# Optimization experiments

Measured on AMD Instinct MI355X. Metric: run time of the kernel, lower is better.

The kernel has to match this reference:

```python
import jax, jax.numpy as jnp
import numpy as np

L = 3          # num encoder layers
H = 128        # hidden_dim
NH = 8         # num_heads
HD = H // NH   # head_dim
FF = H * 4     # ff inner dim (after GLU)
B, N = 32, 512
NUM_BINS = 50


def _linear_params(key, fan_in, fan_out):
    kw, kb = jax.random.split(key)
    lim = 1.0 / np.sqrt(fan_in)
    W = jax.random.uniform(kw, (fan_in, fan_out), jnp.float32, -lim, lim)
    b = jax.random.uniform(kb, (fan_out,), jnp.float32, -lim, lim)
    return W, b


def setup_inputs() -> dict:
    key = jax.random.key(0)
    ks = jax.random.split(key, 16)
    x = jax.random.normal(ks[0], (B, N, H), jnp.float32)
    distance_matrix = jax.random.uniform(ks[1], (B, N, N), jnp.float32)
    mask = jax.random.randint(ks[2], (B, N), 0, 2).astype(bool)

    def stack_linear(k, fan_in, fan_out):
        Ws, bs = [], []
        for l in range(L):
            W, b = _linear_params(jax.random.fold_in(k, l), fan_in, fan_out)
            Ws.append(W); bs.append(b)
        return jnp.stack(Ws), jnp.stack(bs)

    Wq, bq = stack_linear(ks[3], H, H)
    Wk, bk = stack_linear(ks[4], H, H)
    Wv, bv = stack_linear(ks[5], H, H)
    Wo, bo = stack_linear(ks[6], H, H)
    dist_emb = jax.random.normal(ks[7], (L, NUM_BINS, NH), jnp.float32)
    attn_bias = jnp.zeros((L, NH, 1, 1), jnp.float32)
    g1 = jnp.ones((L, H), jnp.float32); b1 = jnp.zeros((L, H), jnp.float32)
    g2 = jnp.ones((L, H), jnp.float32); b2 = jnp.zeros((L, H), jnp.float32)
    Wf1, bf1 = stack_linear(ks[8], H, 2 * FF)
    Wf2, bf2 = stack_linear(ks[9], FF, H)
    return dict(x=x, distance_matrix=distance_matrix, mask=mask,
                Wq=Wq, bq=bq, Wk=Wk, bk=bk, Wv=Wv, bv=bv, Wo=Wo, bo=bo,
                dist_emb=dist_emb, attn_bias=attn_bias,
                g1=g1, b1=b1, g2=g2, b2=b2,
                Wf1=Wf1, bf1=bf1, Wf2=Wf2, bf2=bf2)


def _layernorm(x, g, b, eps=1e-5):
    mu = jnp.mean(x, axis=-1, keepdims=True)
    var = jnp.var(x, axis=-1, keepdims=True)
    return (x - mu) * jax.lax.rsqrt(var + eps) * g + b


def _attention(h, bins, key_mask, Wq, bq, Wk, bk, Wv, bv, Wo, bo, dist_emb, attn_bias):
    # h: [B,N,H]; bins: [B,N,N] int; key_mask: [B,N] bool (True = masked)
    Bsz, Nn, _ = h.shape
    Q = (h @ Wq + bq).reshape(Bsz, Nn, NH, HD)
    K = (h @ Wk + bk).reshape(Bsz, Nn, NH, HD)
    V = (h @ Wv + bv).reshape(Bsz, Nn, NH, HD)
    scores = jnp.einsum('bqhd,bkhd->bhqk', Q, K) / np.sqrt(HD)
    bias = jnp.transpose(dist_emb[bins], (0, 3, 1, 2))  # [B,NH,N,N]
    scores = scores + bias + attn_bias[None]
    scores = jnp.where(key_mask[:, None, None, :], -1e9, scores)
    attn = jax.nn.softmax(scores, axis=-1)
    out = jnp.einsum('bhqk,bkhd->bqhd', attn, V).reshape(Bsz, Nn, H)
    return out @ Wo + bo


def reference(x, distance_matrix, mask, Wq, bq, Wk, bk, Wv, bv, Wo, bo,
              dist_emb, attn_bias, g1, b1, g2, b2, Wf1, bf1, Wf2, bf2):
    bins = jnp.clip((distance_matrix * 10.0).astype(jnp.int32), 0, NUM_BINS - 1)
    h = x
    for l in range(L):
        # pre-LN attention block
        a = _attention(_layernorm(h, g1[l], b1[l]), bins, mask,
                       Wq[l], bq[l], Wk[l], bk[l], Wv[l], bv[l], Wo[l], bo[l],
                       dist_emb[l], attn_bias[l])
        h = h + a
        # pre-LN GLU feed-forward
        u = _layernorm(h, g2[l], b2[l]) @ Wf1[l] + bf1[l]  # [B,N,2*FF]
        ua, ub = jnp.split(u, 2, axis=-1)
        h = h + (ua * jax.nn.sigmoid(ub)) @ Wf2[l] + bf2[l]
    return h
```

## Files before the change

kernel.cpp:

```cpp
#include <hip/hip_runtime.h>
#include <stdint.h>

#define Bq 32
#define Nq 512
#define Hq 128
#define NHq 8
#define HDq 16
#define Mq (Bq * Nq)

typedef unsigned short u16;
typedef __attribute__((ext_vector_type(8))) short short8;
typedef __attribute__((ext_vector_type(8))) _Float16 half8;
typedef __attribute__((ext_vector_type(2))) __fp16 fp16x2;
typedef __attribute__((ext_vector_type(4))) float f32x4;

__device__ __forceinline__ float bf2f(u16 v) {
    return __uint_as_float(((unsigned int)v) << 16);
}
__device__ __forceinline__ float ldin(const void* p, long idx, int bf) {
    if (bf) return bf2f(((const u16*)p)[idx]);
    return ((const float*)p)[idx];
}
__device__ __forceinline__ u16 f2bf(float v) {
    unsigned int u = __float_as_uint(v);
    return (u16)((u + 0x7FFFu + ((u >> 16) & 1u)) >> 16);
}
__device__ __forceinline__ u16 f2h(float v) {
    _Float16 h = (_Float16)v;
    return *(u16*)&h;
}
__device__ __forceinline__ unsigned pk2h(float a, float b) {
    fp16x2 c = __builtin_amdgcn_cvt_pkrtz(a, b);
    return *(unsigned*)&c;
}

__global__ void prep_kernel(const void* xraw, const void* de, const void* ab,
                            const void* mraw, int* flag, float* deo, float* abo,
                            unsigned* mbits, int n) {
    __shared__ int cnt, orA, orB, orC, orD;
    int tid = threadIdx.x;
    if (tid == 0) { cnt = 0; orA = 0; orB = 0; orC = 0; orD = 0; }
    __syncthreads();
    const u16* u = (const u16*)xraw;
    int good = 0;
    for (int i = tid; i < 1024; i += 256) {
        u16 v = u[i];
        int e = (v >> 7) & 0xFF;
        if (v == 0 || (e >= 90 && e <= 141)) good++;
    }
    atomicAdd(&cnt, good);
    const uint4* p4 = (const uint4*)mraw;
    unsigned a = 0, b = 0, c = 0, d = 0;
    for (int i = tid; i < n / 16; i += 256) {
        uint4 w = p4[i];
        unsigned all = w.x | w.y | w.z | w.w;
        a |= all & 0xFEFEFEFEu;
        b |= all & 0x0000FF00u;
        c |= all & 0xFFFFFF00u;
        d |= w.y | w.w;
    }
    if (a) atomicOr(&orA, 1);
    if (b) atomicOr(&orB, 1);
    if (c) atomicOr(&orC, 1);
    if (d) atomicOr(&orD, 1);
    __syncthreads();
    int bf = (cnt >= 900);
    if (tid == 0) *flag = bf;
    int mode;
    if (orA) mode = orB ? 3 : 4;
    else if (orC) mode = 0;
    else mode = orD ? 1 : 2;
    for (int i = tid; i < 1200; i += 256) deo[i] = ldin(de, i, bf);
    if (tid < 24) abo[tid] = ldin(ab, tid, bf);
    const unsigned char* p = (const unsigned char*)mraw;
    for (int wI = tid; wI < n / 32; wI += 256) {
        unsigned word = 0;
        for (int j = 0; j < 32; ++j) {
            int i = wI * 32 + j;
            int v;
            switch (mode) {
                case 0: v = p[i]; break;
                case 1: v = ((const int*)p)[i]; break;
                case 2: v = (int)((const long long*)p)[i]; break;
                case 3: v = ((const u16*)p)[i] != 0; break;
                default: v = (((const float*)p)[i] != 0.0f); break;
            }
            if (v) word |= 1u << j;
        }
        mbits[wI] = word;
    }
}

__global__ void kprep_kernel(const unsigned* __restrict__ mbits,
                             u16* __restrict__ kidxg, int* __restrict__ nkt,
                             unsigned* __restrict__ tmask) {
    int b = blockIdx.x;
    int lane = threadIdx.x & 63;
    int pos_base = 0;
    for (int w = 0; w < 8; ++w) {
        unsigned lo = mbits[b * 16 + 2 * w], hi = mbits[b * 16 + 2 * w + 1];
        unsigned long long word = ((unsigned long long)hi << 32) | lo;
        unsigned long long un = ~word;
        int bit = (int)((un >> lane) & 1ull);
        unsigned long long before = un & ((1ull << lane) - 1ull);
        int pos = pos_base + __popcll(before);
        if (bit) kidxg[b * 512 + pos] = (u16)(w * 64 + lane);
        pos_base += __popcll(un);
    }
    int nk = pos_base;
    int nkp = (nk + 31) & ~31;
    if (nkp == 0) nkp = 32;
    int nt = nkp >> 5;
    for (int j = nk + lane; j < nkp; j += 64) kidxg[b * 512 + j] = 0;
    if (lane == 0) {
        nkt[b] = nt;
        for (int t = 0; t < 16; ++t) tmask[b * 16 + t] = 0;
        int rem = nk & 31;
        if (rem) tmask[b * 16 + nt - 1] = 0xFFFFFFFFu << rem;
        if (nk == 0) tmask[b * 16] = 0xFFFFFFFFu;
    }
}

__global__ __launch_bounds__(256) void binsc_kernel(
    const void* __restrict__ dist, const u16* __restrict__ kidxg,
    const int* __restrict__ nkt, unsigned char* __restrict__ binsc,
    const int* flagp) {
    int bf = *flagp;
    int b = blockIdx.y;
    int q0 = blockIdx.x * 8;
    __shared__ u16 kl[512];
    __shared__ int ntS;
    int tid = threadIdx.x;
    if (tid == 0) ntS = nkt[b];
    kl[tid] = kidxg[b * 512 + tid];
    kl[tid + 256] = kidxg[b * 512 + tid + 256];
    __syncthreads();
    int nkp = ntS * 32;
    for (int rq = 0; rq < 8; ++rq) {
        int q = q0 + rq;
        long rowoff = ((long)b * 512 + q) * 512;
        for (int j = tid; j < nkp; j += 256) {
            float d = ldin(dist, rowoff + kl[j], bf);
            int v = (int)(d * 10.0f);
            v = v < 0 ? 0 : (v > 49 ? 49 : v);
            binsc[((size_t)b * 512 + q) * 512 + j] = (unsigned char)(v << 2);
        }
    }
}

__global__ __launch_bounds__(256) void init_ln_kernel(
    const void* x, float* __restrict__ h, u16* __restrict__ hn,
    const void* graw, const void* braw, const int* flagp) {
    int bf = *flagp;
    int row = blockIdx.x * 4 + (threadIdx.x >> 6);
    int lane = threadIdx.x & 63;
    float x0 = ldin(x, (long)row * Hq + lane, bf);
    float x1 = ldin(x, (long)row * Hq + lane + 64, bf);
    h[(size_t)row * Hq + lane] = x0;
    h[(size_t)row * Hq + lane + 64] = x1;
    float s = x0 + x1, s2 = x0 * x0 + x1 * x1;
#pragma unroll
    for (int o = 32; o; o >>= 1) {
        s += __shfl_xor(s, o);
        s2 += __shfl_xor(s2, o);
    }
    float mu = s * (1.0f / 128.0f);
    float var = fmaxf(s2 * (1.0f / 128.0f) - mu * mu, 0.0f);
    float rr = rsqrtf(var + 1e-5f);
    float g0 = ldin(graw, lane, bf), g1v = ldin(graw, lane + 64, bf);
    float b0 = ldin(braw, lane, bf), b1v = ldin(braw, lane + 64, bf);
    hn[(size_t)row * Hq + lane]      = f2bf((x0 - mu) * rr * g0 + b0);
    hn[(size_t)row * Hq + lane + 64] = f2bf((x1 - mu) * rr * g1v + b1v);
}

__global__ __launch_bounds__(256) void wtrans_kernel(
    const void* Wqr, const void* Wkr, const void* Wvr, const void* Wor,
    const void* Wf1r, const void* Wf2r,
    u16* qkvT, u16* oT, u16* f1T, u16* f2T, const int* flagp) {
    int bf = *flagp;
    int bid = blockIdx.x;
    int l = bid >> 8, r = bid & 255;
    const void* src; u16* dst; long soff, doff; int Kd, Nd, t;
    if (r < 64) {
        int mat = r >> 4; t = r & 15; Kd = 128; Nd = 128;
        soff = (long)l * 16384;
        if (mat == 0)      { src = Wqr; dst = qkvT; doff = (long)l * 49152; }
        else if (mat == 1) { src = Wkr; dst = qkvT; doff = (long)l * 49152 + 16384; }
        else if (mat == 2) { src = Wvr; dst = qkvT; doff = (long)l * 49152 + 32768; }
        else               { src = Wor; dst = oT;   doff = (long)l * 16384; }
    } else if (r < 192) {
        t = r - 64; Kd = 128; Nd = 1024;
        src = Wf1r; soff = (long)l * 131072; dst = f1T; doff = (long)l * 131072;
    } else {
        t = r - 192; Kd = 512; Nd = 128;
        src = Wf2r; soff = (long)l * 65536; dst = f2T; doff = (long)l * 65536;
    }
    int ntile = Nd >> 5;
    int tk = t / ntile, tn = t % ntile;
    __shared__ u16 Ts[32][33];
    int rr = threadIdx.x >> 3, cc0 = (threadIdx.x & 7) * 4;
#pragma unroll
    for (int i = 0; i < 4; ++i) {
        long idx = soff + (long)(tk * 32 + rr) * Nd + tn * 32 + cc0 + i;
        Ts[rr][cc0 + i] = f2bf(ldin(src, idx, bf));
    }
    __syncthreads();
#pragma unroll
    for (int i = 0; i < 4; ++i) {
        long idx = doff + (long)(tn * 32 + rr) * Kd + tk * 32 + cc0 + i;
        dst[idx] = Ts[cc0 + i][rr];
    }
}

__global__ __launch_bounds__(256, 2) void mfma_gemm64_kernel(
    const u16* __restrict__ A, const u16* __restrict__ WT,
    const void* __restrict__ braw, long bOff, float* __restrict__ C,
    int K, int resid, const int* flagp,
    const void* lnG, const void* lnB, long lnOff, u16* hnout, void* outp) {
    __shared__ __align__(16) u16 As[64][40];
    __shared__ __align__(16) u16 Bs[128][40];
    __shared__ float Ct[64][128];
    int tid = threadIdx.x;
    int m0 = blockIdx.x * 64;
    int wave = tid >> 6, lane = tid & 63;
    int wm = (wave >> 1) * 32, wn = (wave & 1) * 64;
    int q = lane >> 4, ln = lane & 15;
    f32x4 zero = {0.f, 0.f, 0.f, 0.f};
    f32x4 acc[2][4];
#pragma unroll
    for (int i = 0; i < 2; ++i)
#pragma unroll
        for (int j = 0; j < 4; ++j) acc[i][j] = zero;
    int sar = tid >> 2, sac = (tid & 3) * 8;
    int sbr = tid >> 1, sbc = (tid & 1) * 16;
    const u16* Ap = A + (size_t)(m0 + sar) * K + sac;
    const u16* Bp = WT + (size_t)sbr * K + sbc;
    for (int k0 = 0; k0 < K; k0 += 32) {
        uint4 av = *(const uint4*)(Ap + k0);
        uint4 b0 = *(const uint4*)(Bp + k0);
        uint4 b1 = *(const uint4*)(Bp + k0 + 8);
        *(uint4*)&As[sar][sac] = av;
        *(uint4*)&Bs[sbr][sbc] = b0; *(uint4*)&Bs[sbr][sbc + 8] = b1;
        __syncthreads();
        short8 af[2], bfv[4];
#pragma unroll
        for (int t = 0; t < 2; ++t) af[t] = *(const short8*)&As[wm + t * 16 + ln][q * 8];
#pragma unroll
        for (int t = 0; t < 4; ++t) bfv[t] = *(const short8*)&Bs[wn + t * 16 + ln][q * 8];
#pragma unroll
        for (int ti = 0; ti < 2; ++ti)
#pragma unroll
            for (int tj = 0; tj < 4; ++tj)
                acc[ti][tj] = __builtin_amdgcn_mfma_f32_16x16x32_bf16(
                    af[ti], bfv[tj], acc[ti][tj], 0, 0, 0);
        __syncthreads();
    }
    int bf = *flagp;
#pragma unroll
    for (int tj = 0; tj < 4; ++tj) {
        int n = wn + tj * 16 + ln;
        float bias = ldin(braw, bOff + n, bf);
#pragma unroll
        for (int ti = 0; ti < 2; ++ti)
#pragma unroll
            for (int r = 0; r < 4; ++r) {
                int m = m0 + wm + ti * 16 + q * 4 + r;
                float v = acc[ti][tj][r] + bias;
                float* dst = C + (size_t)m * 128 + n;
                if (resid) v += *dst;
                *dst = v;
                Ct[m - m0][n] = v;
                if (outp) {
                    if (bf) ((u16*)outp)[(size_t)m * 128 + n] = f2bf(v);
                    else ((float*)outp)[(size_t)m * 128 + n] = v;
                }
            }
    }
    if (hnout) {
        __syncthreads();
        float gg0 = ldin(lnG, lnOff + lane, bf);
        float gg1 = ldin(lnG, lnOff + lane + 64, bf);
        float bb0 = ldin(lnB, lnOff + lane, bf);
        float bb1 = ldin(lnB, lnOff + lane + 64, bf);
        for (int rr = 0; rr < 16; ++rr) {
            int row = wave * 16 + rr;
            float x0 = Ct[row][lane], x1 = Ct[row][lane + 64];
            float s = x0 + x1, s2v = x0 * x0 + x1 * x1;
#pragma unroll
            for (int o = 32; o; o >>= 1) {
                s += __shfl_xor(s, o);
                s2v += __shfl_xor(s2v, o);
            }
            float mu = s * (1.0f / 128.0f);
            float var = fmaxf(s2v * (1.0f / 128.0f) - mu * mu, 0.0f);
            float rstd = rsqrtf(var + 1e-5f);
            int m = m0 + row;
            hnout[(size_t)m * 128 + lane]      = f2bf((x0 - mu) * rstd * gg0 + bb0);
            hnout[(size_t)m * 128 + lane + 64] = f2bf((x1 - mu) * rstd * gg1 + bb1);
        }
    }
}

__global__ __launch_bounds__(256, 2) void qkv_mfma_kernel(
    const u16* __restrict__ A, const u16* __restrict__ qkvT_l,
    const void* bqr, const void* bkr, const void* bvr, long bOff,
    u16* __restrict__ Qo, u16* __restrict__ Ko, u16* __restrict__ Vo,
    const int* flagp) {
    int sel = blockIdx.y;
    const u16* WT = qkvT_l + (size_t)sel * 16384;
    const void* braw = sel == 0 ? bqr : (sel == 1 ? bkr : bvr);
    u16* C = sel == 0 ? Qo : (sel == 1 ? Ko : Vo);
    float scale = sel == 0 ? 0.25f : 1.0f;
    __shared__ __align__(16) u16 As[64][40];
    __shared__ __align__(16) u16 Bs[128][40];
    int tid = threadIdx.x;
    int m0 = blockIdx.x * 64;
    int wave = tid >> 6, lane = tid & 63;
    int wm = (wave >> 1) * 32, wn = (wave & 1) * 64;
    int q = lane >> 4, ln = lane & 15;
    f32x4 zero = {0.f, 0.f, 0.f, 0.f};
    f32x4 acc[2][4];
#pragma unroll
    for (int i = 0; i < 2; ++i)
#pragma unroll
        for (int j = 0; j < 4; ++j) acc[i][j] = zero;
    int sar = tid >> 2, sac = (tid & 3) * 8;
    int sbr = tid >> 1, sbc = (tid & 1) * 16;
    const u16* Ap = A + (size_t)(m0 + sar) * 128 + sac;
    const u16* Bp = WT + (size_t)sbr * 128 + sbc;
#pragma unroll
    for (int k0 = 0; k0 < 128; k0 += 32) {
        uint4 av = *(const uint4*)(Ap + k0);
        uint4 b0 = *(const uint4*)(Bp + k0);
        uint4 b1 = *(const uint4*)(Bp + k0 + 8);
        *(uint4*)&As[sar][sac] = av;
        *(uint4*)&Bs[sbr][sbc] = b0; *(uint4*)&Bs[sbr][sbc + 8] = b1;
        __syncthreads();
        short8 af[2], bfv[4];
#pragma unroll
        for (int t = 0; t < 2; ++t) af[t] = *(const short8*)&As[wm + t * 16 + ln][q * 8];
#pragma unroll
        for (int t = 0; t < 4; ++t) bfv[t] = *(const short8*)&Bs[wn + t * 16 + ln][q * 8];
#pragma unroll
        for (int ti = 0; ti < 2; ++ti)
#pragma unroll
            for (int tj = 0; tj < 4; ++tj)
                acc[ti][tj] = __builtin_amdgcn_mfma_f32_16x16x32_bf16(
                    af[ti], bfv[tj], acc[ti][tj], 0, 0, 0);
        __syncthreads();
    }
    int bf = *flagp;
#pragma unroll
    for (int tj = 0; tj < 4; ++tj) {
        int n = wn + tj * 16 + ln;
        float bias = ldin(braw, bOff + n, bf);
#pragma unroll
        for (int ti = 0; ti < 2; ++ti)
#pragma unroll
            for (int r = 0; r < 4; ++r) {
                int m = m0 + wm + ti * 16 + q * 4 + r;
                C[(size_t)m * 128 + n] = f2h((acc[ti][tj][r] + bias) * scale);
            }
    }
}

__global__ __launch_bounds__(256, 2) void glu_mfma_kernel(
    const u16* __restrict__ A, const u16* __restrict__ f1T_l,
    const void* __restrict__ braw, long bOff, u16* __restrict__ Vout,
    const int* flagp) {
    __shared__ __align__(16) u16 As[128][40];
    __shared__ __align__(16) u16 Ba[64][40];
    __shared__ __align__(16) u16 Bb[64][40];
    int tid = threadIdx.x;
    int m0 = blockIdx.x * 128, n0 = blockIdx.y * 64;
    int wave = tid >> 6, lane = tid & 63;
    int wm = (wave >> 1) * 64, wn = (wave & 1) * 32;
    int q = lane >> 4, ln = lane & 15;
    f32x4 zero = {0.f, 0.f, 0.f, 0.f};
    f32x4 accA[4][2], accB[4][2];
#pragma unroll
    for (int i = 0; i < 4; ++i)
#pragma unroll
        for (int j = 0; j < 2; ++j) { accA[i][j] = zero; accB[i][j] = zero; }
    int sr = tid >> 1, sc = (tid & 1) * 16;
    const u16* Ap = A + (size_t)(m0 + sr) * 128 + sc;
    const u16* BpA = f1T_l + (size_t)(n0 + sr) * 128 + sc;
    const u16* BpB = f1T_l + (size_t)(512 + n0 + (sr - 64)) * 128 + sc;
#pragma unroll
    for (int k0 = 0; k0 < 128; k0 += 32) {
        uint4 a0 = *(const uint4*)(Ap + k0);
        uint4 a1 = *(const uint4*)(Ap + k0 + 8);
        *(uint4*)&As[sr][sc] = a0; *(uint4*)&As[sr][sc + 8] = a1;
        if (sr < 64) {
            uint4 w0 = *(const uint4*)(BpA + k0);
            uint4 w1 = *(const uint4*)(BpA + k0 + 8);
            *(uint4*)&Ba[sr][sc] = w0; *(uint4*)&Ba[sr][sc + 8] = w1;
        } else {
            uint4 w0 = *(const uint4*)(BpB + k0);
            uint4 w1 = *(const uint4*)(BpB + k0 + 8);
            *(uint4*)&Bb[sr - 64][sc] = w0; *(uint4*)&Bb[sr - 64][sc + 8] = w1;
        }
        __syncthreads();
        short8 af[4], ba[2], bb[2];
#pragma unroll
        for (int t = 0; t < 4; ++t) af[t] = *(const short8*)&As[wm + t * 16 + ln][q * 8];
#pragma unroll
        for (int t = 0; t < 2; ++t) {
            ba[t] = *(const short8*)&Ba[wn + t * 16 + ln][q * 8];
            bb[t] = *(const short8*)&Bb[wn + t * 16 + ln][q * 8];
        }
#pragma unroll
        for (int ti = 0; ti < 4; ++ti)
#pragma unroll
            for (int tj = 0; tj < 2; ++tj) {
                accA[ti][tj] = __builtin_amdgcn_mfma_f32_16x16x32_bf16(
                    af[ti], ba[tj], accA[ti][tj], 0, 0, 0);
                accB[ti][tj] = __builtin_amdgcn_mfma_f32_16x16x32_bf16(
                    af[ti], bb[tj], accB[ti][tj], 0, 0, 0);
            }
        __syncthreads();
    }
    int bf = *flagp;
#pragma unroll
    for (int tj = 0; tj < 2; ++tj) {
        int n = n0 + wn + tj * 16 + ln;
        float biasA = ldin(braw, bOff + n, bf);
        float biasB = ldin(braw, bOff + 512 + n, bf);
#pragma unroll
        for (int ti = 0; ti < 4; ++ti)
#pragma unroll
            for (int r = 0; r < 4; ++r) {
                int m = m0 + wm + ti * 16 + q * 4 + r;
                float ua = accA[ti][tj][r] + biasA;
                float ub = accB[ti][tj][r] + biasB;
                Vout[(size_t)m * 512 + n] = f2bf(ua / (1.0f + __expf(-ub)));
            }
    }
}

__global__ __launch_bounds__(256, 4) void attn_kernel(
    const u16* __restrict__ Qh, const u16* __restrict__ Kh,
    const u16* __restrict__ Vh, const unsigned char* __restrict__ binsc,
    const u16* __restrict__ kidxg, const int* __restrict__ nktp,
    const unsigned* __restrict__ tmaskp, const float* __restrict__ deL,
    const float* __restrict__ abL, u16* __restrict__ out) {
    int id = blockIdx.x;
    int c = id & 7, t5 = id >> 3;
    int nh = t5 & 7;
    int pair = ((t5 >> 3) << 3) | c;
    int b = pair >> 2, qq = pair & 3;

    __shared__ __align__(16) u16 KsF[8192];
    __shared__ __align__(16) u16 VT[16 * 520];
    __shared__ __align__(16) u16 Pl[4 * 16 * 40];

    int tid = threadIdx.x;
    int nt = __builtin_amdgcn_readfirstlane(nktp[b]);
    int nkp = nt * 32;
    const u16* Kp = Kh + (size_t)(b * Nq) * Hq + nh * HDq;
    const u16* Vp = Vh + (size_t)(b * Nq) * Hq + nh * HDq;
    for (int r = tid; r < nkp; r += 256) {
        int row = kidxg[b * 512 + r];
        int kt = r >> 5, s = (r >> 4) & 1, lnr = r & 15;
        uint4 k0v = *(const uint4*)(Kp + (size_t)row * Hq);
        uint4 k1v = *(const uint4*)(Kp + (size_t)row * Hq + 8);
        *(uint4*)&KsF[kt * 512 + s * 256 + lnr * 8]       = k0v;
        *(uint4*)&KsF[kt * 512 + s * 256 + 128 + lnr * 8] = k1v;
        uint4 v0 = *(const uint4*)(Vp + (size_t)row * Hq);
        uint4 v1 = *(const uint4*)(Vp + (size_t)row * Hq + 8);
        u16 vv[16];
        *(uint4*)&vv[0] = v0; *(uint4*)&vv[8] = v1;
#pragma unroll
        for (int d = 0; d < 16; ++d) VT[d * 520 + r] = vv[d];
    }
    __syncthreads();

    int wave = tid >> 6, lane = tid & 63;
    int quad = lane >> 4, ln = lane & 15;
    int q0w = qq * 128 + wave * 32;

    float tblf = (lane < 50) ? deL[lane * NHq + nh] + abL[nh] : 0.0f;
    int tbli = __float_as_int(tblf);
    unsigned tl = tmaskp[b * 16 + nt - 1];

    half8 qf[2];
#pragma unroll
    for (int t = 0; t < 2; ++t) {
        uint4 qv = {0, 0, 0, 0};
        if (quad < 2)
            qv = *(const uint4*)(Qh + (size_t)(b * Nq + q0w + t * 16 + ln) * Hq
                                 + nh * HDq + quad * 8);
        qf[t] = *(half8*)&qv;
    }

    f32x4 zero = {0.f, 0.f, 0.f, 0.f};
    f32x4 acc[2] = {zero, zero};
    float zp[2] = {0.f, 0.f};
    _Float16* Pw = (_Float16*)&Pl[wave * 640];
    const _Float16* KsH = (const _Float16*)KsF;
    const _Float16* VTH = (const _Float16*)VT;
    const unsigned char* brow0 = binsc + ((size_t)b * 512 + (q0w + ln)) * 512;
    const unsigned char* brow1 = brow0 + (size_t)16 * 512;

    unsigned pb00 = *(const unsigned*)(brow0 + quad * 4);
    unsigned pb01 = *(const unsigned*)(brow0 + 16 + quad * 4);
    unsigned pb10 = *(const unsigned*)(brow1 + quad * 4);
    unsigned pb11 = *(const unsigned*)(brow1 + 16 + quad * 4);

    for (int kt = 0; kt < nt; ++kt) {
        int k0 = kt * 32;
        unsigned w = (kt == nt - 1) ? tl : 0u;
        unsigned cb00 = pb00, cb01 = pb01, cb10 = pb10, cb11 = pb11;
        if (kt < nt - 1) {
            pb00 = *(const unsigned*)(brow0 + k0 + 32 + quad * 4);
            pb01 = *(const unsigned*)(brow0 + k0 + 48 + quad * 4);
            pb10 = *(const unsigned*)(brow1 + k0 + 32 + quad * 4);
            pb11 = *(const unsigned*)(brow1 + k0 + 48 + quad * 4);
        }
        half8 vb = *(const half8*)(VTH + ln * 520 + k0 + quad * 8);
        half8 ka0 = {}, ka1 = {};
        if (quad < 2) {
            ka0 = *(const half8*)(KsH + kt * 512 + quad * 128 + ln * 8);
            ka1 = *(const half8*)(KsH + kt * 512 + 256 + quad * 128 + ln * 8);
        }
#pragma unroll
        for (int t = 0; t < 2; ++t) {
            unsigned bw0 = t == 0 ? cb00 : cb10;
            unsigned bw1 = t == 0 ? cb01 : cb11;
            f32x4 s0 = __builtin_amdgcn_mfma_f32_16x16x32_f16(ka0, qf[t], zero, 0, 0, 0);
            f32x4 s1 = __builtin_amdgcn_mfma_f32_16x16x32_f16(ka1, qf[t], zero, 0, 0, 0);
            float p[8];
#pragma unroll
            for (int r = 0; r < 4; ++r) {
                float bias = __int_as_float(__builtin_amdgcn_ds_bpermute(
                    (int)((bw0 >> (8 * r)) & 0xFFu), tbli));
                float sc = s0[r] + bias;
                bool m = (w >> (quad * 4 + r)) & 1u;
                p[r] = m ? 0.0f : __expf(sc);
            }
#pragma unroll
            for (int r = 0; r < 4; ++r) {
                float bias = __int_as_float(__builtin_amdgcn_ds_bpermute(
                    (int)((bw1 >> (8 * r)) & 0xFFu), tbli));
                float sc = s1[r] + bias;
                bool m = (w >> (16 + quad * 4 + r)) & 1u;
                p[4 + r] = m ? 0.0f : __expf(sc);
            }
            zp[t] += ((p[0] + p[1]) + (p[2] + p[3])) +
                     ((p[4] + p[5]) + (p[6] + p[7]));
            uint2 w0, w1;
            w0.x = pk2h(p[0], p[1]); w0.y = pk2h(p[2], p[3]);
            w1.x = pk2h(p[4], p[5]); w1.y = pk2h(p[6], p[7]);
            *(uint2*)(Pw + ln * 40 + quad * 4)      = w0;
            *(uint2*)(Pw + ln * 40 + 16 + quad * 4) = w1;
            half8 pa = *(const half8*)(Pw + ln * 40 + quad * 8);
            acc[t] = __builtin_amdgcn_mfma_f32_16x16x32_f16(pa, vb, acc[t], 0, 0, 0);
        }
    }
#pragma unroll
    for (int t = 0; t < 2; ++t) {
        zp[t] += __shfl_xor(zp[t], 16);
        zp[t] += __shfl_xor(zp[t], 32);
    }
#pragma unroll
    for (int t = 0; t < 2; ++t) {
#pragma unroll
        for (int r = 0; r < 4; ++r) {
            float zz = __shfl(zp[t], quad * 4 + r);
            float val = acc[t][r] / fmaxf(zz, 1e-35f);
            int qrow = q0w + t * 16 + quad * 4 + r;
            out[(size_t)(b * Nq + qrow) * Hq + nh * HDq + ln] = f2bf(val);
        }
    }
}

extern "C" void kernel_launch(void* const* d_in, const int* in_sizes, int n_in,
                              void* d_out, int out_size, void* d_ws, size_t ws_size,
                              hipStream_t stream) {
    const void* x  = d_in[0];
    const void* dist = d_in[1];
    const void* mask = d_in[2];
    const void* Wq = d_in[3];  const void* bq = d_in[4];
    const void* Wk = d_in[5];  const void* bk = d_in[6];
    const void* Wv = d_in[7];  const void* bv = d_in[8];
    const void* Wo = d_in[9];  const void* bo = d_in[10];
    const void* de = d_in[11]; const void* ab = d_in[12];
    const void* g1 = d_in[13]; const void* b1 = d_in[14];
    const void* g2 = d_in[15]; const void* b2 = d_in[16];
    const void* Wf1 = d_in[17]; const void* bf1 = d_in[18];
    const void* Wf2 = d_in[19]; const void* bf2 = d_in[20];

    char* ws = (char*)d_ws;
    const size_t OFF_DE   = 64;
    const size_t OFF_AB   = 5120;
    const size_t OFF_BINS = 8192;
    const size_t OFF_MSK  = OFF_BINS + 8388608;
    const size_t OFF_KIDX = OFF_MSK + 4096;
    const size_t OFF_NKT  = OFF_KIDX + 32768;
    const size_t OFF_TM   = OFF_NKT + 256;
    const size_t OFF_H    = OFF_TM + 4096;
    const size_t OFF_QKV  = OFF_H + 8388608;
    const size_t OFF_HN   = OFF_QKV + 25165824;
    const size_t OFF_ATT  = OFF_HN + 4194304;
    const size_t OFF_WT   = OFF_ATT + 4194304;
    const size_t NEEDED   = OFF_WT + 1572864;
    if (ws_size < NEEDED) return;

    int* flag = (int*)ws;
    float* deF = (float*)(ws + OFF_DE);
    float* abF = (float*)(ws + OFF_AB);
    unsigned char* binsc = (unsigned char*)(ws + OFF_BINS);
    unsigned* mbits = (unsigned*)(ws + OFF_MSK);
    u16* kidxg = (u16*)(ws + OFF_KIDX);
    int* nkt = (int*)(ws + OFF_NKT);
    unsigned* tmask = (unsigned*)(ws + OFF_TM);
    float* h = (float*)(ws + OFF_H);
    u16* Qh = (u16*)(ws + OFF_QKV);
    u16* Kh = Qh + 2097152;
    u16* Vh = Qh + 2 * 2097152;
    u16* vglu = (u16*)(ws + OFF_QKV);
    u16* hn = (u16*)(ws + OFF_HN);
    u16* att = (u16*)(ws + OFF_ATT);
    u16* qkvT = (u16*)(ws + OFF_WT);
    u16* oT  = qkvT + 147456;
    u16* f1T = oT + 49152;
    u16* f2T = f1T + 393216;

    prep_kernel<<<1, 256, 0, stream>>>(x, de, ab, mask, flag, deF, abF, mbits, Bq * Nq);
    kprep_kernel<<<32, 64, 0, stream>>>(mbits, kidxg, nkt, tmask);
    dim3 gbc(64, 32);
    binsc_kernel<<<gbc, 256, 0, stream>>>(dist, kidxg, nkt, binsc, flag);
    init_ln_kernel<<<4096, 256, 0, stream>>>(x, h, hn, g1, b1, flag);
    wtrans_kernel<<<768, 256, 0, stream>>>(Wq, Wk, Wv, Wo, Wf1, Wf2,
                                           qkvT, oT, f1T, f2T, flag);

    dim3 gqkv(256, 3);
    dim3 gglu(128, 8);
    for (int l = 0; l < 3; ++l) {
        qkv_mfma_kernel<<<gqkv, 256, 0, stream>>>(hn, qkvT + (size_t)l * 49152,
                                                  bq, bk, bv, (long)l * Hq,
                                                  Qh, Kh, Vh, flag);
        attn_kernel<<<1024, 256, 0, stream>>>(Qh, Kh, Vh, binsc, kidxg, nkt, tmask,
                                              deF + (long)l * 400, abF + (long)l * 8, att);
        mfma_gemm64_kernel<<<256, 256, 0, stream>>>(att, oT + (size_t)l * 16384,
                                                    bo, (long)l * Hq, h, 128, 1, flag,
                                                    g2, b2, (long)l * Hq, hn, nullptr);
        glu_mfma_kernel<<<gglu, 256, 0, stream>>>(hn, f1T + (size_t)l * 131072,
                                                  bf1, (long)l * 1024, vglu, flag);
        if (l < 2) {
            mfma_gemm64_kernel<<<256, 256, 0, stream>>>(vglu, f2T + (size_t)l * 65536,
                                                        bf2, (long)l * Hq, h, 512, 1, flag,
                                                        g1, b1, (long)(l + 1) * Hq, hn,
                                                        nullptr);
        } else {
            mfma_gemm64_kernel<<<256, 256, 0, stream>>>(vglu, f2T + (size_t)l * 65536,
                                                        bf2, (long)l * Hq, h, 512, 1, flag,
                                                        nullptr, nullptr, 0, nullptr,
                                                        d_out);
        }
    }
}
```

Before: 407.0 us.

## Merge setup kernels and stage full K-slab tiles in GEMM kernels

Folds the key-index prep into the single-block prep kernel, and merges bin computation, initial layernorm and weight transposition into one combined launch dispatched by block index. This removes several kernel launches. The QKV, GLU and output GEMM kernels now load the whole K range (or 256-wide slabs) into shared memory at once instead of 32-wide steps, which cuts the number of barriers per tile. The cost is much larger LDS footprint per block, so occupancy drops; launch bounds are adjusted to match.

```diff
diff --git a/kernel.cpp b/kernel.cpp
--- a/kernel.cpp
+++ b/kernel.cpp
@@ -36,8 +36,11 @@
 
 __global__ void prep_kernel(const void* xraw, const void* de, const void* ab,
                             const void* mraw, int* flag, float* deo, float* abo,
-                            unsigned* mbits, int n) {
+                            unsigned* mbits, int n,
+                            u16* __restrict__ kidxg, int* __restrict__ nkt,
+                            unsigned* __restrict__ tmask) {
     __shared__ int cnt, orA, orB, orC, orD;
+    __shared__ unsigned smb[512];
     int tid = threadIdx.x;
     if (tid == 0) { cnt = 0; orA = 0; orB = 0; orC = 0; orD = 0; }
     __syncthreads();
@@ -88,137 +91,131 @@
             if (v) word |= 1u << j;
         }
         mbits[wI] = word;
-    }
-}
-
-__global__ void kprep_kernel(const unsigned* __restrict__ mbits,
-                             u16* __restrict__ kidxg, int* __restrict__ nkt,
-                             unsigned* __restrict__ tmask) {
-    int b = blockIdx.x;
-    int lane = threadIdx.x & 63;
-    int pos_base = 0;
-    for (int w = 0; w < 8; ++w) {
-        unsigned lo = mbits[b * 16 + 2 * w], hi = mbits[b * 16 + 2 * w + 1];
-        unsigned long long word = ((unsigned long long)hi << 32) | lo;
-        unsigned long long un = ~word;
-        int bit = (int)((un >> lane) & 1ull);
-        unsigned long long before = un & ((1ull << lane) - 1ull);
-        int pos = pos_base + __popcll(before);
-        if (bit) kidxg[b * 512 + pos] = (u16)(w * 64 + lane);
-        pos_base += __popcll(un);
-    }
-    int nk = pos_base;
-    int nkp = (nk + 31) & ~31;
-    if (nkp == 0) nkp = 32;
-    int nt = nkp >> 5;
-    for (int j = nk + lane; j < nkp; j += 64) kidxg[b * 512 + j] = 0;
-    if (lane == 0) {
-        nkt[b] = nt;
-        for (int t = 0; t < 16; ++t) tmask[b * 16 + t] = 0;
-        int rem = nk & 31;
-        if (rem) tmask[b * 16 + nt - 1] = 0xFFFFFFFFu << rem;
-        if (nk == 0) tmask[b * 16] = 0xFFFFFFFFu;
-    }
-}
-
-__global__ __launch_bounds__(256) void binsc_kernel(
+        smb[wI] = word;
+    }
+    __syncthreads();
+    int lane = tid & 63;
+    for (int bb = tid >> 6; bb < 32; bb += 4) {
+        int pos_base = 0;
+        for (int w = 0; w < 8; ++w) {
+            unsigned lo = smb[bb * 16 + 2 * w], hi = smb[bb * 16 + 2 * w + 1];
+            unsigned long long word = ((unsigned long long)hi << 32) | lo;
+            unsigned long long un = ~word;
+            int bit = (int)((un >> lane) & 1ull);
+            unsigned long long before = un & ((1ull << lane) - 1ull);
+            int pos = pos_base + __popcll(before);
+            if (bit) kidxg[bb * 512 + pos] = (u16)(w * 64 + lane);
+            pos_base += __popcll(un);
+        }
+        int nk = pos_base;
+        int nkp = (nk + 31) & ~31;
+        if (nkp == 0) nkp = 32;
+        int nt = nkp >> 5;
+        for (int j = nk + lane; j < nkp; j += 64) kidxg[bb * 512 + j] = 0;
+        if (lane == 0) {
+            nkt[bb] = nt;
+            for (int t = 0; t < 16; ++t) tmask[bb * 16 + t] = 0;
+            int rem = nk & 31;
+            if (rem) tmask[bb * 16 + nt - 1] = 0xFFFFFFFFu << rem;
+            if (nk == 0) tmask[bb * 16] = 0xFFFFFFFFu;
+        }
+    }
+}
+
+__global__ __launch_bounds__(256) void setup2_kernel(
     const void* __restrict__ dist, const u16* __restrict__ kidxg,
-    const int* __restrict__ nkt, unsigned char* __restrict__ binsc,
-    const int* flagp) {
-    int bf = *flagp;
-    int b = blockIdx.y;
-    int q0 = blockIdx.x * 8;
-    __shared__ u16 kl[512];
-    __shared__ int ntS;
-    int tid = threadIdx.x;
-    if (tid == 0) ntS = nkt[b];
-    kl[tid] = kidxg[b * 512 + tid];
-    kl[tid + 256] = kidxg[b * 512 + tid + 256];
-    __syncthreads();
-    int nkp = ntS * 32;
-    for (int rq = 0; rq < 8; ++rq) {
-        int q = q0 + rq;
-        long rowoff = ((long)b * 512 + q) * 512;
-        for (int j = tid; j < nkp; j += 256) {
-            float d = ldin(dist, rowoff + kl[j], bf);
-            int v = (int)(d * 10.0f);
-            v = v < 0 ? 0 : (v > 49 ? 49 : v);
-            binsc[((size_t)b * 512 + q) * 512 + j] = (unsigned char)(v << 2);
-        }
-    }
-}
-
-__global__ __launch_bounds__(256) void init_ln_kernel(
+    const int* __restrict__ nktp, unsigned char* __restrict__ binsc,
     const void* x, float* __restrict__ h, u16* __restrict__ hn,
-    const void* graw, const void* braw, const int* flagp) {
-    int bf = *flagp;
-    int row = blockIdx.x * 4 + (threadIdx.x >> 6);
-    int lane = threadIdx.x & 63;
-    float x0 = ldin(x, (long)row * Hq + lane, bf);
-    float x1 = ldin(x, (long)row * Hq + lane + 64, bf);
-    h[(size_t)row * Hq + lane] = x0;
-    h[(size_t)row * Hq + lane + 64] = x1;
-    float s = x0 + x1, s2 = x0 * x0 + x1 * x1;
-#pragma unroll
-    for (int o = 32; o; o >>= 1) {
-        s += __shfl_xor(s, o);
-        s2 += __shfl_xor(s2, o);
-    }
-    float mu = s * (1.0f / 128.0f);
-    float var = fmaxf(s2 * (1.0f / 128.0f) - mu * mu, 0.0f);
-    float rr = rsqrtf(var + 1e-5f);
-    float g0 = ldin(graw, lane, bf), g1v = ldin(graw, lane + 64, bf);
-    float b0 = ldin(braw, lane, bf), b1v = ldin(braw, lane + 64, bf);
-    hn[(size_t)row * Hq + lane]      = f2bf((x0 - mu) * rr * g0 + b0);
-    hn[(size_t)row * Hq + lane + 64] = f2bf((x1 - mu) * rr * g1v + b1v);
-}
-
-__global__ __launch_bounds__(256) void wtrans_kernel(
+    const void* g1raw, const void* b1raw,
     const void* Wqr, const void* Wkr, const void* Wvr, const void* Wor,
     const void* Wf1r, const void* Wf2r,
     u16* qkvT, u16* oT, u16* f1T, u16* f2T, const int* flagp) {
+    __shared__ u16 kl[512];
+    __shared__ int ntS;
+    __shared__ u16 Ts[32][33];
+    int id = blockIdx.x;
+    int tid = threadIdx.x;
     int bf = *flagp;
-    int bid = blockIdx.x;
-    int l = bid >> 8, r = bid & 255;
-    const void* src; u16* dst; long soff, doff; int Kd, Nd, t;
-    if (r < 64) {
-        int mat = r >> 4; t = r & 15; Kd = 128; Nd = 128;
-        soff = (long)l * 16384;
-        if (mat == 0)      { src = Wqr; dst = qkvT; doff = (long)l * 49152; }
-        else if (mat == 1) { src = Wkr; dst = qkvT; doff = (long)l * 49152 + 16384; }
-        else if (mat == 2) { src = Wvr; dst = qkvT; doff = (long)l * 49152 + 32768; }
-        else               { src = Wor; dst = oT;   doff = (long)l * 16384; }
-    } else if (r < 192) {
-        t = r - 64; Kd = 128; Nd = 1024;
-        src = Wf1r; soff = (long)l * 131072; dst = f1T; doff = (long)l * 131072;
+    if (id < 2048) {
+        int b = id >> 6;
+        int q0 = (id & 63) * 8;
+        if (tid == 0) ntS = nktp[b];
+        kl[tid] = kidxg[b * 512 + tid];
+        kl[tid + 256] = kidxg[b * 512 + tid + 256];
+        __syncthreads();
+        int nkp = ntS * 32;
+        for (int rq = 0; rq < 8; ++rq) {
+            int q = q0 + rq;
+            long rowoff = ((long)b * 512 + q) * 512;
+            for (int j = tid; j < nkp; j += 256) {
+                float d = ldin(dist, rowoff + kl[j], bf);
+                int v = (int)(d * 10.0f);
+                v = v < 0 ? 0 : (v > 49 ? 49 : v);
+                binsc[((size_t)b * 512 + q) * 512 + j] = (unsigned char)(v << 2);
+            }
+        }
+    } else if (id < 6144) {
+        int row = (id - 2048) * 4 + (tid >> 6);
+        int lane = tid & 63;
+        float x0 = ldin(x, (long)row * Hq + lane, bf);
+        float x1 = ldin(x, (long)row * Hq + lane + 64, bf);
+        h[(size_t)row * Hq + lane] = x0;
+        h[(size_t)row * Hq + lane + 64] = x1;
+        float s = x0 + x1, s2 = x0 * x0 + x1 * x1;
+#pragma unroll
+        for (int o = 32; o; o >>= 1) {
+            s += __shfl_xor(s, o);
+            s2 += __shfl_xor(s2, o);
+        }
+        float mu = s * (1.0f / 128.0f);
+        float var = fmaxf(s2 * (1.0f / 128.0f) - mu * mu, 0.0f);
+        float rr = rsqrtf(var + 1e-5f);
+        float g0 = ldin(g1raw, lane, bf), g1v = ldin(g1raw, lane + 64, bf);
+        float b0 = ldin(b1raw, lane, bf), b1v = ldin(b1raw, lane + 64, bf);
+        hn[(size_t)row * Hq + lane]      = f2bf((x0 - mu) * rr * g0 + b0);
+        hn[(size_t)row * Hq + lane + 64] = f2bf((x1 - mu) * rr * g1v + b1v);
     } else {
-        t = r - 192; Kd = 512; Nd = 128;
-        src = Wf2r; soff = (long)l * 65536; dst = f2T; doff = (long)l * 65536;
-    }
-    int ntile = Nd >> 5;
-    int tk = t / ntile, tn = t % ntile;
-    __shared__ u16 Ts[32][33];
-    int rr = threadIdx.x >> 3, cc0 = (threadIdx.x & 7) * 4;
-#pragma unroll
-    for (int i = 0; i < 4; ++i) {
-        long idx = soff + (long)(tk * 32 + rr) * Nd + tn * 32 + cc0 + i;
-        Ts[rr][cc0 + i] = f2bf(ldin(src, idx, bf));
-    }
-    __syncthreads();
-#pragma unroll
-    for (int i = 0; i < 4; ++i) {
-        long idx = doff + (long)(tn * 32 + rr) * Kd + tk * 32 + cc0 + i;
-        dst[idx] = Ts[cc0 + i][rr];
-    }
-}
-
-__global__ __launch_bounds__(256, 2) void mfma_gemm64_kernel(
+        int bid = id - 6144;
+        int l = bid >> 8, r = bid & 255;
+        const void* src; u16* dst; long soff, doff; int Kd, Nd, t;
+        if (r < 64) {
+            int mat = r >> 4; t = r & 15; Kd = 128; Nd = 128;
+            soff = (long)l * 16384;
+            if (mat == 0)      { src = Wqr; dst = qkvT; doff = (long)l * 49152; }
+            else if (mat == 1) { src = Wkr; dst = qkvT; doff = (long)l * 49152 + 16384; }
+            else if (mat == 2) { src = Wvr; dst = qkvT; doff = (long)l * 49152 + 32768; }
+            else               { src = Wor; dst = oT;   doff = (long)l * 16384; }
+        } else if (r < 192) {
+            t = r - 64; Kd = 128; Nd = 1024;
+            src = Wf1r; soff = (long)l * 131072; dst = f1T; doff = (long)l * 131072;
+        } else {
+            t = r - 192; Kd = 512; Nd = 128;
+            src = Wf2r; soff = (long)l * 65536; dst = f2T; doff = (long)l * 65536;
+        }
+        int ntile = Nd >> 5;
+        int tk = t / ntile, tn = t % ntile;
+        int rr = tid >> 3, cc0 = (tid & 7) * 4;
+#pragma unroll
+        for (int i = 0; i < 4; ++i) {
+            long idx = soff + (long)(tk * 32 + rr) * Nd + tn * 32 + cc0 + i;
+            Ts[rr][cc0 + i] = f2bf(ldin(src, idx, bf));
+        }
+        __syncthreads();
+#pragma unroll
+        for (int i = 0; i < 4; ++i) {
+            long idx = doff + (long)(tn * 32 + rr) * Kd + tk * 32 + cc0 + i;
+            dst[idx] = Ts[cc0 + i][rr];
+        }
+    }
+}
+
+__global__ __launch_bounds__(256, 1) void mfma_gemm64_kernel(
     const u16* __restrict__ A, const u16* __restrict__ WT,
     const void* __restrict__ braw, long bOff, float* __restrict__ C,
     int K, int resid, const int* flagp,
     const void* lnG, const void* lnB, long lnOff, u16* hnout, void* outp) {
-    __shared__ __align__(16) u16 As[64][40];
-    __shared__ __align__(16) u16 Bs[128][40];
+    __shared__ __align__(16) u16 As[64][264];
+    __shared__ __align__(16) u16 Bs[128][264];
     __shared__ float Ct[64][128];
     int tid = threadIdx.x;
     int m0 = blockIdx.x * 64;
@@ -231,28 +228,34 @@
     for (int i = 0; i < 2; ++i)
 #pragma unroll
         for (int j = 0; j < 4; ++j) acc[i][j] = zero;
-    int sar = tid >> 2, sac = (tid & 3) * 8;
-    int sbr = tid >> 1, sbc = (tid & 1) * 16;
-    const u16* Ap = A + (size_t)(m0 + sar) * K + sac;
-    const u16* Bp = WT + (size_t)sbr * K + sbc;
-    for (int k0 = 0; k0 < K; k0 += 32) {
-        uint4 av = *(const uint4*)(Ap + k0);
-        uint4 b0 = *(const uint4*)(Bp + k0);
-        uint4 b1 = *(const uint4*)(Bp + k0 + 8);
-        *(uint4*)&As[sar][sac] = av;
-        *(uint4*)&Bs[sbr][sbc] = b0; *(uint4*)&Bs[sbr][sbc + 8] = b1;
+    for (int k0 = 0; k0 < K; k0 += 256) {
+        int ks = K - k0; if (ks > 256) ks = 256;
+        int sh = (ks == 256) ? 5 : 4;
+        int cm = (1 << sh) - 1;
+        for (int idx = tid; idx < (64 << sh); idx += 256) {
+            int r = idx >> sh, c = (idx & cm) << 3;
+            *(uint4*)&As[r][c] = *(const uint4*)(A + (size_t)(m0 + r) * K + k0 + c);
+        }
+        for (int idx = tid; idx < (128 << sh); idx += 256) {
+            int r = idx >> sh, c = (idx & cm) << 3;
+            *(uint4*)&Bs[r][c] = *(const uint4*)(WT + (size_t)r * K + k0 + c);
+        }
         __syncthreads();
-        short8 af[2], bfv[4];
-#pragma unroll
-        for (int t = 0; t < 2; ++t) af[t] = *(const short8*)&As[wm + t * 16 + ln][q * 8];
-#pragma unroll
-        for (int t = 0; t < 4; ++t) bfv[t] = *(const short8*)&Bs[wn + t * 16 + ln][q * 8];
-#pragma unroll
-        for (int ti = 0; ti < 2; ++ti)
-#pragma unroll
-            for (int tj = 0; tj < 4; ++tj)
-                acc[ti][tj] = __builtin_amdgcn_mfma_f32_16x16x32_bf16(
-                    af[ti], bfv[tj], acc[ti][tj], 0, 0, 0);
+        for (int kf = 0; kf < ks; kf += 32) {
+            short8 af[2], bfv[4];
+#pragma unroll
+            for (int t = 0; t < 2; ++t)
+                af[t] = *(const short8*)&As[wm + t * 16 + ln][kf + q * 8];
+#pragma unroll
+            for (int t = 0; t < 4; ++t)
+                bfv[t] = *(const short8*)&Bs[wn + t * 16 + ln][kf + q * 8];
+#pragma unroll
+            for (int ti = 0; ti < 2; ++ti)
+#pragma unroll
+                for (int tj = 0; tj < 4; ++tj)
+                    acc[ti][tj] = __builtin_amdgcn_mfma_f32_16x16x32_bf16(
+                        af[ti], bfv[tj], acc[ti][tj], 0, 0, 0);
+        }
         __syncthreads();
     }
     int bf = *flagp;
@@ -301,7 +304,7 @@
     }
 }
 
-__global__ __launch_bounds__(256, 2) void qkv_mfma_kernel(
+__global__ __launch_bounds__(256, 3) void qkv_mfma_kernel(
     const u16* __restrict__ A, const u16* __restrict__ qkvT_l,
     const void* bqr, const void* bkr, const void* bvr, long bOff,
     u16* __restrict__ Qo, u16* __restrict__ Ko, u16* __restrict__ Vo,
@@ -311,8 +314,8 @@
     const void* braw = sel == 0 ? bqr : (sel == 1 ? bkr : bvr);
     u16* C = sel == 0 ? Qo : (sel == 1 ? Ko : Vo);
     float scale = sel == 0 ? 0.25f : 1.0f;
-    __shared__ __align__(16) u16 As[64][40];
-    __shared__ __align__(16) u16 Bs[128][40];
+    __shared__ __align__(16) u16 As[64][136];
+    __shared__ __align__(16) u16 Bs[128][136];
     int tid = threadIdx.x;
     int m0 = blockIdx.x * 64;
     int wave = tid >> 6, lane = tid & 63;
@@ -324,30 +327,34 @@
     for (int i = 0; i < 2; ++i)
 #pragma unroll
         for (int j = 0; j < 4; ++j) acc[i][j] = zero;
-    int sar = tid >> 2, sac = (tid & 3) * 8;
-    int sbr = tid >> 1, sbc = (tid & 1) * 16;
-    const u16* Ap = A + (size_t)(m0 + sar) * 128 + sac;
-    const u16* Bp = WT + (size_t)sbr * 128 + sbc;
-#pragma unroll
-    for (int k0 = 0; k0 < 128; k0 += 32) {
-        uint4 av = *(const uint4*)(Ap + k0);
-        uint4 b0 = *(const uint4*)(Bp + k0);
-        uint4 b1 = *(const uint4*)(Bp + k0 + 8);
-        *(uint4*)&As[sar][sac] = av;
-        *(uint4*)&Bs[sbr][sbc] = b0; *(uint4*)&Bs[sbr][sbc + 8] = b1;
-        __syncthreads();
+#pragma unroll
+    for (int i = 0; i < 4; ++i) {
+        int idx = tid + i * 256;
+        int r = idx >> 4, c = (idx & 15) << 3;
+        *(uint4*)&As[r][c] = *(const uint4*)(A + (size_t)(m0 + r) * 128 + c);
+    }
+#pragma unroll
+    for (int i = 0; i < 8; ++i) {
+        int idx = tid + i * 256;
+        int r = idx >> 4, c = (idx & 15) << 3;
+        *(uint4*)&Bs[r][c] = *(const uint4*)(WT + (size_t)r * 128 + c);
+    }
+    __syncthreads();
+#pragma unroll
+    for (int kf = 0; kf < 128; kf += 32) {
         short8 af[2], bfv[4];
 #pragma unroll
-        for (int t = 0; t < 2; ++t) af[t] = *(const short8*)&As[wm + t * 16 + ln][q * 8];
-#pragma unroll
-        for (int t = 0; t < 4; ++t) bfv[t] = *(const short8*)&Bs[wn + t * 16 + ln][q * 8];
+        for (int t = 0; t < 2; ++t)
+            af[t] = *(const short8*)&As[wm + t * 16 + ln][kf + q * 8];
+#pragma unroll
+        for (int t = 0; t < 4; ++t)
+            bfv[t] = *(const short8*)&Bs[wn + t * 16 + ln][kf + q * 8];
 #pragma unroll
         for (int ti = 0; ti < 2; ++ti)
 #pragma unroll
             for (int tj = 0; tj < 4; ++tj)
                 acc[ti][tj] = __builtin_amdgcn_mfma_f32_16x16x32_bf16(
                     af[ti], bfv[tj], acc[ti][tj], 0, 0, 0);
-        __syncthreads();
     }
     int bf = *flagp;
 #pragma unroll
@@ -368,9 +375,9 @@
     const u16* __restrict__ A, const u16* __restrict__ f1T_l,
     const void* __restrict__ braw, long bOff, u16* __restrict__ Vout,
     const int* flagp) {
-    __shared__ __align__(16) u16 As[128][40];
-    __shared__ __align__(16) u16 Ba[64][40];
-    __shared__ __align__(16) u16 Bb[64][40];
+    __shared__ __align__(16) u16 As[128][136];
+    __shared__ __align__(16) u16 Ba[64][136];
+    __shared__ __align__(16) u16 Bb[64][136];
     int tid = threadIdx.x;
     int m0 = blockIdx.x * 128, n0 = blockIdx.y * 64;
     int wave = tid >> 6, lane = tid & 63;
@@ -382,32 +389,30 @@
     for (int i = 0; i < 4; ++i)
 #pragma unroll
         for (int j = 0; j < 2; ++j) { accA[i][j] = zero; accB[i][j] = zero; }
-    int sr = tid >> 1, sc = (tid & 1) * 16;
-    const u16* Ap = A + (size_t)(m0 + sr) * 128 + sc;
-    const u16* BpA = f1T_l + (size_t)(n0 + sr) * 128 + sc;
-    const u16* BpB = f1T_l + (size_t)(512 + n0 + (sr - 64)) * 128 + sc;
-#pragma unroll
-    for (int k0 = 0; k0 < 128; k0 += 32) {
-        uint4 a0 = *(const uint4*)(Ap + k0);
-        uint4 a1 = *(const uint4*)(Ap + k0 + 8);
-        *(uint4*)&As[sr][sc] = a0; *(uint4*)&As[sr][sc + 8] = a1;
-        if (sr < 64) {
-            uint4 w0 = *(const uint4*)(BpA + k0);
-            uint4 w1 = *(const uint4*)(BpA + k0 + 8);
-            *(uint4*)&Ba[sr][sc] = w0; *(uint4*)&Ba[sr][sc + 8] = w1;
-        } else {
-            uint4 w0 = *(const uint4*)(BpB + k0);
-            uint4 w1 = *(const uint4*)(BpB + k0 + 8);
-            *(uint4*)&Bb[sr - 64][sc] = w0; *(uint4*)&Bb[sr - 64][sc + 8] = w1;
-        }
-        __syncthreads();
+#pragma unroll
+    for (int i = 0; i < 8; ++i) {
+        int idx = tid + i * 256;
+        int r = idx >> 4, c = (idx & 15) << 3;
+        *(uint4*)&As[r][c] = *(const uint4*)(A + (size_t)(m0 + r) * 128 + c);
+    }
+#pragma unroll
+    for (int i = 0; i < 4; ++i) {
+        int idx = tid + i * 256;
+        int r = idx >> 4, c = (idx & 15) << 3;
+        *(uint4*)&Ba[r][c] = *(const uint4*)(f1T_l + (size_t)(n0 + r) * 128 + c);
+        *(uint4*)&Bb[r][c] = *(const uint4*)(f1T_l + (size_t)(512 + n0 + r) * 128 + c);
+    }
+    __syncthreads();
+#pragma unroll
+    for (int kf = 0; kf < 128; kf += 32) {
         short8 af[4], ba[2], bb[2];
 #pragma unroll
-        for (int t = 0; t < 4; ++t) af[t] = *(const short8*)&As[wm + t * 16 + ln][q * 8];
+        for (int t = 0; t < 4; ++t)
+            af[t] = *(const short8*)&As[wm + t * 16 + ln][kf + q * 8];
 #pragma unroll
         for (int t = 0; t < 2; ++t) {
-            ba[t] = *(const short8*)&Ba[wn + t * 16 + ln][q * 8];
-            bb[t] = *(const short8*)&Bb[wn + t * 16 + ln][q * 8];
+            ba[t] = *(const short8*)&Ba[wn + t * 16 + ln][kf + q * 8];
+            bb[t] = *(const short8*)&Bb[wn + t * 16 + ln][kf + q * 8];
         }
 #pragma unroll
         for (int ti = 0; ti < 4; ++ti)
@@ -418,7 +423,6 @@
                 accB[ti][tj] = __builtin_amdgcn_mfma_f32_16x16x32_bf16(
                     af[ti], bb[tj], accB[ti][tj], 0, 0, 0);
             }
-        __syncthreads();
     }
     int bf = *flagp;
 #pragma unroll
@@ -626,13 +630,12 @@
     u16* f1T = oT + 49152;
     u16* f2T = f1T + 393216;
 
-    prep_kernel<<<1, 256, 0, stream>>>(x, de, ab, mask, flag, deF, abF, mbits, Bq * Nq);
-    kprep_kernel<<<32, 64, 0, stream>>>(mbits, kidxg, nkt, tmask);
-    dim3 gbc(64, 32);
-    binsc_kernel<<<gbc, 256, 0, stream>>>(dist, kidxg, nkt, binsc, flag);
-    init_ln_kernel<<<4096, 256, 0, stream>>>(x, h, hn, g1, b1, flag);
-    wtrans_kernel<<<768, 256, 0, stream>>>(Wq, Wk, Wv, Wo, Wf1, Wf2,
-                                           qkvT, oT, f1T, f2T, flag);
+    prep_kernel<<<1, 256, 0, stream>>>(x, de, ab, mask, flag, deF, abF, mbits,
+                                       Bq * Nq, kidxg, nkt, tmask);
+    setup2_kernel<<<6912, 256, 0, stream>>>(dist, kidxg, nkt, binsc,
+                                            x, h, hn, g1, b1,
+                                            Wq, Wk, Wv, Wo, Wf1, Wf2,
+                                            qkvT, oT, f1T, f2T, flag);
 
     dim3 gqkv(256, 3);
     dim3 gglu(128, 8);
```

After: 433.4 us. 1.06x slower.
